# Optimization experiments

Hardware: AMD Instinct MI355X
Metric: run time of the kernel (lower is better)

The kernel has to match this reference:

```python
import jax, jax.numpy as jnp
import numpy as np

N_HEADS = 16
D_HEAD = 64


def setup_inputs() -> dict:
    key = jax.random.key(0)
    ks = jax.random.split(key, 9)
    B, n, L, Lt = 2, 8, 4096, 77
    d, ctx = 1024, 768
    H = W = 64
    s = 0.02  # weight init scale for numerical sanity
    return {
        "x": jax.random.normal(ks[0], (B, L, d), jnp.float32),
        "reorg_masks": jax.random.uniform(ks[1], (B, n, H, W), jnp.float32),
        "text_feat": jax.random.normal(ks[2], (B, n, Lt, ctx), jnp.float32),
        "Wq": jax.random.normal(ks[3], (d, d), jnp.float32) * s,
        "Wk": jax.random.normal(ks[4], (ctx, d), jnp.float32) * s,
        "Wv": jax.random.normal(ks[5], (ctx, d), jnp.float32) * s,
        "Wo": jax.random.normal(ks[6], (d, d), jnp.float32) * s,
        "bo": jax.random.normal(ks[7], (d,), jnp.float32) * s,
        "null_text_feat": jax.random.normal(ks[8], (d,), jnp.float32) * s,
    }


def _cross_attention(xf, ctx, Wq, Wk, Wv, Wo, bo):
    # xf: (BN, L, d), ctx: (BN, Lt, c)
    BN, L, _ = xf.shape
    Lt = ctx.shape[1]
    q = (xf @ Wq).reshape(BN, L, N_HEADS, D_HEAD)
    k = (ctx @ Wk).reshape(BN, Lt, N_HEADS, D_HEAD)
    v = (ctx @ Wv).reshape(BN, Lt, N_HEADS, D_HEAD)
    scale = 1.0 / np.sqrt(D_HEAD).astype(np.float32)
    logits = jnp.einsum("blhd,bthd->bhlt", q, k) * scale
    attn = jax.nn.softmax(logits, axis=-1)
    out = jnp.einsum("bhlt,bthd->blhd", attn, v).reshape(BN, L, N_HEADS * D_HEAD)
    return out @ Wo + bo


def reference(x, reorg_masks, text_feat, Wq, Wk, Wv, Wo, bo, null_text_feat):
    B, L, d = x.shape
    n = reorg_masks.shape[1]
    # masks are already at (H, W) with H*W == L, so nearest interp is identity
    x_flat = jnp.broadcast_to(x[:, None], (B, n, L, d)).reshape(B * n, L, d)
    ctx_flat = text_feat.reshape(B * n, text_feat.shape[2], text_feat.shape[3])
    x_obj = _cross_attention(x_flat, ctx_flat, Wq, Wk, Wv, Wo, bo)
    x_obj = x_obj.reshape(B, n, L, d)
    region = jnp.where(reorg_masks > 0.5, 1.0, 0.0).astype(x.dtype)
    region = region.reshape(B, n, L, 1)  # (b, n, h*w, 1)
    x_sum = jnp.sum(x_obj * region, axis=1)  # (B, L, d)
    cover = jnp.sum(region, axis=1)  # (B, L, 1)
    x_null = (1.0 - cover) * null_text_feat[None, None, :]
    return x_sum + x_null + x
```

## Files before the change

### kernel.cpp

```cpp
#include <hip/hip_runtime.h>


typedef __bf16 bf16;
typedef __bf16 bf16x8 __attribute__((ext_vector_type(8)));
typedef __bf16 bf16x4 __attribute__((ext_vector_type(4)));
typedef float  f32x4  __attribute__((ext_vector_type(4)));

#define MFMA16(a, b, c) __builtin_amdgcn_mfma_f32_16x16x32_bf16((a), (b), (c), 0, 0, 0)


__device__ inline bf16x8 cvt8(const float* p) {
  f32x4 a = *(const f32x4*)p;
  f32x4 b = *(const f32x4*)(p + 4);
  bf16x8 r;
  r[0] = (bf16)a[0]; r[1] = (bf16)a[1]; r[2] = (bf16)a[2]; r[3] = (bf16)a[3];
  r[4] = (bf16)b[0]; r[5] = (bf16)b[1]; r[6] = (bf16)b[2]; r[7] = (bf16)b[3];
  return r;
}

__global__ __launch_bounds__(256) void transpose_all(
    const float* __restrict__ Wq, const float* __restrict__ Wk,
    const float* __restrict__ Wv, const float* __restrict__ Wo,
    bf16* __restrict__ WqT, bf16* __restrict__ WkT,
    bf16* __restrict__ WvT, bf16* __restrict__ WoT,
    const float* __restrict__ mask, float* __restrict__ cover) {
  __shared__ bf16 tile[32][33];
  int bx = blockIdx.x;
  int byg = blockIdx.y;
  if (byg == 112) {
    int tid = bx * 256 + threadIdx.x;
    int b = tid >> 12, l = tid & 4095;
    float c = 0.f;
#pragma unroll
    for (int n = 0; n < 8; n++)
      c += (mask[(size_t)(b * 8 + n) * 4096 + l] > 0.5f) ? 1.f : 0.f;
    cover[tid] = c;
    return;
  }
  int tx = threadIdx.x & 31, ty = threadIdx.x >> 5;
  const float* in;
  bf16* out;
  int R, by;
  if (byg < 32)      { in = Wq; out = WqT; R = 1024; by = byg; }
  else if (byg < 56) { in = Wk; out = WkT; R = 768;  by = byg - 32; }
  else if (byg < 80) { in = Wv; out = WvT; R = 768;  by = byg - 56; }
  else               { in = Wo; out = WoT; R = 1024; by = byg - 80; }
  const int C = 1024;
  int c = bx * 32 + tx;
#pragma unroll
  for (int i = 0; i < 32; i += 8) {
    int r = by * 32 + ty + i;
    tile[ty + i][tx] = (bf16)in[(size_t)r * C + c];
  }
  __syncthreads();
#pragma unroll
  for (int i = 0; i < 32; i += 8) {
    out[(size_t)(bx * 32 + ty + i) * R + by * 32 + tx] = tile[tx][ty + i];
  }
}

__device__ __forceinline__ void gemm_q_body(const float* __restrict__ A,
                                            const bf16* __restrict__ BT,
                                            bf16* __restrict__ C,
                                            int bx, int by) {
  __shared__ __align__(16) bf16 asA[2][64 * 32];
  const int tid = threadIdx.x;
  const int lane = tid & 63, wave = tid >> 6;
  const int l16 = lane & 15, quad = lane >> 4;
  const int m0 = by * 64;
  const int n0 = bx * 256 + wave * 64;
  const int srow = tid >> 2, scol = (tid & 3) * 8;
  const float* aptr = A + (size_t)(m0 + srow) * 1024 + scol;

  *(bf16x8*)(&asA[0][srow * 32 + scol]) = cvt8(aptr);

  f32x4 acc[4][4];
#pragma unroll
  for (int i = 0; i < 4; i++)
#pragma unroll
    for (int j = 0; j < 4; j++)
#pragma unroll
      for (int r = 0; r < 4; r++) acc[i][j][r] = 0.f;

  for (int kt = 0; kt < 32; kt++) {
    bf16x8 wnext;
    if (kt + 1 < 32) wnext = cvt8(aptr + (kt + 1) * 32);
    __syncthreads();
    const bf16* ab = &asA[kt & 1][0];
    bf16x8 a[4], b[4];
#pragma unroll
    for (int mi = 0; mi < 4; mi++)
      a[mi] = *(const bf16x8*)(ab + (mi * 16 + l16) * 32 + quad * 8);
#pragma unroll
    for (int ni = 0; ni < 4; ni++)
      b[ni] = *(const bf16x8*)(BT + (size_t)(n0 + ni * 16 + l16) * 1024 + kt * 32 + quad * 8);
#pragma unroll
    for (int mi = 0; mi < 4; mi++)
#pragma unroll
      for (int ni = 0; ni < 4; ni++) acc[mi][ni] = MFMA16(a[mi], b[ni], acc[mi][ni]);
    if (kt + 1 < 32)
      *(bf16x8*)(&asA[(kt + 1) & 1][srow * 32 + scol]) = wnext;
  }

#pragma unroll
  for (int mi = 0; mi < 4; mi++)
#pragma unroll
    for (int r = 0; r < 4; r++) {
      int row = m0 + mi * 16 + quad * 4 + r;
#pragma unroll
      for (int ni = 0; ni < 4; ni++)
        C[(size_t)row * 1024 + n0 + ni * 16 + l16] = (bf16)(acc[mi][ni][r] * 0.125f);
    }
}

__device__ __forceinline__ void gemm_k_body(const float* __restrict__ text,
                                            const bf16* __restrict__ WkT,
                                            bf16* __restrict__ Kp,
                                            int bx, int bn) {
  const int tid = threadIdx.x;
  const int lane = tid & 63, wave = tid >> 6;
  const int l16 = lane & 15, quad = lane >> 4;
  const int m0 = (wave >> 1) * 64;
  const int n0 = bx * 128 + (wave & 1) * 64;
  const float* A = text + (size_t)bn * 77 * 768;
  bf16* dst = Kp + (size_t)bn * 80 * 1024;

  f32x4 acc[4][4];
#pragma unroll
  for (int i = 0; i < 4; i++)
#pragma unroll
    for (int j = 0; j < 4; j++)
#pragma unroll
      for (int r = 0; r < 4; r++) acc[i][j][r] = 0.f;

  for (int k0 = 0; k0 < 768; k0 += 32) {
    bf16x8 a[4], b[4];
#pragma unroll
    for (int mi = 0; mi < 4; mi++) {
      int row = m0 + mi * 16 + l16;
      if (row >= 77) row = 76;
      a[mi] = cvt8(A + (size_t)row * 768 + k0 + quad * 8);
    }
#pragma unroll
    for (int ni = 0; ni < 4; ni++)
      b[ni] = *(const bf16x8*)(WkT + (size_t)(n0 + ni * 16 + l16) * 768 + k0 + quad * 8);
#pragma unroll
    for (int mi = 0; mi < 4; mi++)
#pragma unroll
      for (int ni = 0; ni < 4; ni++) acc[mi][ni] = MFMA16(a[mi], b[ni], acc[mi][ni]);
  }

#pragma unroll
  for (int mi = 0; mi < 4; mi++)
#pragma unroll
    for (int r = 0; r < 4; r++) {
      int t = m0 + mi * 16 + quad * 4 + r;
      if (t < 77) {
#pragma unroll
        for (int ni = 0; ni < 4; ni++)
          dst[(size_t)t * 1024 + n0 + ni * 16 + l16] = (bf16)acc[mi][ni][r];
      } else if (t < 80) {
#pragma unroll
        for (int ni = 0; ni < 4; ni++)
          dst[(size_t)t * 1024 + n0 + ni * 16 + l16] = (bf16)0.f;
      }
    }
}

__device__ __forceinline__ void gemm_v_body(const float* __restrict__ text,
                                            const bf16* __restrict__ WvT,
                                            bf16* __restrict__ Vt,
                                            int bx, int bn) {
  const int tid = threadIdx.x;
  const int lane = tid & 63, wave = tid >> 6;
  const int l16 = lane & 15, quad = lane >> 4;
  const int m0 = (wave >> 1) * 64;
  const int n0 = bx * 128 + (wave & 1) * 64;
  const float* A = text + (size_t)bn * 77 * 768;
  bf16* dst = Vt + (size_t)bn * 1024 * 96;

  f32x4 acc[4][4];
#pragma unroll
  for (int i = 0; i < 4; i++)
#pragma unroll
    for (int j = 0; j < 4; j++)
#pragma unroll
      for (int r = 0; r < 4; r++) acc[i][j][r] = 0.f;

  for (int k0 = 0; k0 < 768; k0 += 32) {
    bf16x8 a[4], b[4];
#pragma unroll
    for (int mi = 0; mi < 4; mi++) {
      int row = m0 + mi * 16 + l16;
      if (row >= 77) row = 76;
      a[mi] = cvt8(A + (size_t)row * 768 + k0 + quad * 8);
    }
#pragma unroll
    for (int ni = 0; ni < 4; ni++)
      b[ni] = *(const bf16x8*)(WvT + (size_t)(n0 + ni * 16 + l16) * 768 + k0 + quad * 8);
#pragma unroll
    for (int mi = 0; mi < 4; mi++)
#pragma unroll
      for (int ni = 0; ni < 4; ni++) acc[mi][ni] = MFMA16(a[mi], b[ni], acc[mi][ni]);
  }

#pragma unroll
  for (int mi = 0; mi < 4; mi++) {
    int t0 = m0 + mi * 16 + quad * 4;
#pragma unroll
    for (int ni = 0; ni < 4; ni++) {
      int col = n0 + ni * 16 + l16;
      bf16* cbase = dst + (size_t)col * 96;
      if (t0 + 3 < 77) {
        bf16x4 w;
        w[0] = (bf16)acc[mi][ni][0]; w[1] = (bf16)acc[mi][ni][1];
        w[2] = (bf16)acc[mi][ni][2]; w[3] = (bf16)acc[mi][ni][3];
        *(bf16x4*)(cbase + t0) = w;
      } else {
#pragma unroll
        for (int r = 0; r < 4; r++) {
          int t = t0 + r;
          if (t < 77)      cbase[t] = (bf16)acc[mi][ni][r];
          else if (t < 96) cbase[t] = (bf16)0.f;
        }
      }
    }
  }
}

__global__ __launch_bounds__(256) void proj_qkv(const float* __restrict__ x,
                                                const bf16* __restrict__ WqT,
                                                bf16* __restrict__ Qb,
                                                const float* __restrict__ text,
                                                const bf16* __restrict__ WkT,
                                                const bf16* __restrict__ WvT,
                                                bf16* __restrict__ Kp,
                                                bf16* __restrict__ Vt) {
  const int bid = blockIdx.x;
  if (bid < 512) {
    gemm_q_body(x, WqT, Qb, bid & 3, bid >> 2);
  } else {
    const int r = bid - 512;
    const int bx = r & 7, bn = (r >> 3) & 15, kz = r >> 7;
    if (kz == 0) gemm_k_body(text, WkT, Kp, bx, bn);
    else         gemm_v_body(text, WvT, Vt, bx, bn);
  }
}

__global__ __launch_bounds__(256) void gemm_q_f(const float* __restrict__ A,
                                                const bf16* __restrict__ BT,
                                                float* __restrict__ C) {
  __shared__ __align__(16) bf16 asA[2][64 * 32];
  const int tid = threadIdx.x;
  const int lane = tid & 63, wave = tid >> 6;
  const int l16 = lane & 15, quad = lane >> 4;
  const int m0 = blockIdx.y * 64;
  const int n0 = blockIdx.x * 256 + wave * 64;
  const int srow = tid >> 2, scol = (tid & 3) * 8;
  const float* aptr = A + (size_t)(m0 + srow) * 1024 + scol;

  *(bf16x8*)(&asA[0][srow * 32 + scol]) = cvt8(aptr);

  f32x4 acc[4][4];
#pragma unroll
  for (int i = 0; i < 4; i++)
#pragma unroll
    for (int j = 0; j < 4; j++)
#pragma unroll
      for (int r = 0; r < 4; r++) acc[i][j][r] = 0.f;

  for (int kt = 0; kt < 32; kt++) {
    bf16x8 wnext;
    if (kt + 1 < 32) wnext = cvt8(aptr + (kt + 1) * 32);
    __syncthreads();
    const bf16* ab = &asA[kt & 1][0];
    bf16x8 a[4], b[4];
#pragma unroll
    for (int mi = 0; mi < 4; mi++)
      a[mi] = *(const bf16x8*)(ab + (mi * 16 + l16) * 32 + quad * 8);
#pragma unroll
    for (int ni = 0; ni < 4; ni++)
      b[ni] = *(const bf16x8*)(BT + (size_t)(n0 + ni * 16 + l16) * 1024 + kt * 32 + quad * 8);
#pragma unroll
    for (int mi = 0; mi < 4; mi++)
#pragma unroll
      for (int ni = 0; ni < 4; ni++) acc[mi][ni] = MFMA16(a[mi], b[ni], acc[mi][ni]);
    if (kt + 1 < 32) {
      *(bf16x8*)(&asA[(kt + 1) & 1][srow * 32 + scol]) = wnext;
    }
  }

#pragma unroll
  for (int mi = 0; mi < 4; mi++)
#pragma unroll
    for (int r = 0; r < 4; r++) {
      int row = m0 + mi * 16 + quad * 4 + r;
#pragma unroll
      for (int ni = 0; ni < 4; ni++)
        C[(size_t)row * 1024 + n0 + ni * 16 + l16] = acc[mi][ni][r] * 0.125f;
    }
}

template <typename OutT, typename InT>
__device__ __forceinline__ void attn_body(const InT* Qsrc, OutT* Odst,
                                          const bf16* __restrict__ Kp,
                                          const bf16* __restrict__ Vt,
                                          const float* __restrict__ mask) {
  __shared__ __align__(16) bf16 kl[80 * 72];
  __shared__ __align__(16) bf16 vl[64 * 104];
  __shared__ __align__(16) bf16 p_lds[4][16 * 104];
  const int tid = threadIdx.x;
  const int lane = tid & 63, wave = tid >> 6;
  const int l16 = lane & 15, quad = lane >> 4;
  const int bid = blockIdx.x;
  const int qg = bid & 31;
  const int h = (bid >> 5) & 15;
  const int b = bid >> 9;
  const int qrow0 = qg * 128 + wave * 32;
  bf16* pl = &p_lds[wave][0];

  for (int i = lane; i < 16 * 16; i += 64) {
    int r = i >> 4, c = 80 + (i & 15);
    pl[r * 104 + c] = (bf16)0.f;
  }

  bf16x8 qf[2][2];
#pragma unroll
  for (int mi = 0; mi < 2; mi++)
#pragma unroll
    for (int ks = 0; ks < 2; ks++) {
      const InT* qp = Qsrc + (size_t)(b * 4096 + qrow0 + mi * 16 + l16) * 1024 +
                      h * 64 + ks * 32 + quad * 8;
      if constexpr (sizeof(InT) == 4) qf[mi][ks] = cvt8((const float*)qp);
      else                            qf[mi][ks] = *(const bf16x8*)qp;
    }

  unsigned rbits[2];
#pragma unroll
  for (int mi = 0; mi < 2; mi++) {
    unsigned m = 0;
#pragma unroll
    for (int n = 0; n < 8; n++)
      if (mask[(size_t)(b * 8 + n) * 4096 + qrow0 + mi * 16 + l16] > 0.5f)
        m |= (1u << n);
    rbits[mi] = m;
  }

  f32x4 oacc[2][4];
#pragma unroll
  for (int mi = 0; mi < 2; mi++)
#pragma unroll
    for (int nt = 0; nt < 4; nt++)
#pragma unroll
      for (int r = 0; r < 4; r++) oacc[mi][nt][r] = 0.f;

  for (int n = 0; n < 8; n++) {
    const int bn = b * 8 + n;
    const bf16* Ksrc = Kp + (size_t)bn * 80 * 1024 + h * 64;
    const bf16* Vsrc = Vt + (size_t)bn * 1024 * 96 + (size_t)h * 64 * 96;

    for (int i = tid; i < 640; i += 256) {
      int row = i >> 3, c8 = (i & 7) * 8;
      *(bf16x8*)(kl + row * 72 + c8) = *(const bf16x8*)(Ksrc + (size_t)row * 1024 + c8);
    }
    for (int i = tid; i < 768; i += 256) {
      int row = i / 12, c8 = (i % 12) * 8;
      *(bf16x8*)(vl + row * 104 + c8) = *(const bf16x8*)(Vsrc + (size_t)row * 96 + c8);
    }
    __syncthreads();

    f32x4 s[2][5];
#pragma unroll
    for (int mi = 0; mi < 2; mi++)
#pragma unroll
      for (int tt = 0; tt < 5; tt++)
#pragma unroll
        for (int r = 0; r < 4; r++) s[mi][tt][r] = 0.f;

#pragma unroll
    for (int tt = 0; tt < 5; tt++) {
      int t = tt * 16 + l16;
      bf16x8 kf0 = *(const bf16x8*)(kl + t * 72 + quad * 8);
      bf16x8 kf1 = *(const bf16x8*)(kl + t * 72 + 32 + quad * 8);
#pragma unroll
      for (int mi = 0; mi < 2; mi++) {
        s[mi][tt] = MFMA16(kf0, qf[mi][0], s[mi][tt]);
        s[mi][tt] = MFMA16(kf1, qf[mi][1], s[mi][tt]);
      }
    }

#pragma unroll
    for (int mi = 0; mi < 2; mi++) {
      float sum = 0.f;
#pragma unroll
      for (int tt = 0; tt < 5; tt++) {
#pragma unroll
        for (int r = 0; r < 4; r++) {
          float e = __expf(s[mi][tt][r]);
          if (tt == 4 && quad * 4 + r >= 13) e = 0.f;
          s[mi][tt][r] = e;
          sum += e;
        }
      }
      sum += __shfl_xor(sum, 16);
      sum += __shfl_xor(sum, 32);
      float rg = ((rbits[mi] >> n) & 1u) ? 1.f : 0.f;
      float scale = rg / sum;
#pragma unroll
      for (int tt = 0; tt < 5; tt++) {
        bf16x4 w;
#pragma unroll
        for (int r = 0; r < 4; r++) w[r] = (bf16)(s[mi][tt][r] * scale);
        *(bf16x4*)(pl + l16 * 104 + tt * 16 + quad * 4) = w;
      }

#pragma unroll
      for (int ks = 0; ks < 3; ks++) {
        bf16x8 pf = *(const bf16x8*)(pl + l16 * 104 + ks * 32 + quad * 8);
#pragma unroll
        for (int nt = 0; nt < 4; nt++) {
          bf16x8 vf = *(const bf16x8*)(vl + (nt * 16 + l16) * 104 + ks * 32 + quad * 8);
          oacc[mi][nt] = MFMA16(pf, vf, oacc[mi][nt]);
        }
      }
    }
    __syncthreads();
  }

#pragma unroll
  for (int mi = 0; mi < 2; mi++)
#pragma unroll
    for (int r = 0; r < 4; r++) {
      size_t row = (size_t)(b * 4096 + qrow0 + mi * 16 + quad * 4 + r);
#pragma unroll
      for (int nt = 0; nt < 4; nt++)
        Odst[row * 1024 + h * 64 + nt * 16 + l16] = (OutT)oacc[mi][nt][r];
    }
}

__global__ __launch_bounds__(256, 4) void attn_b(const bf16* Qb, bf16* ACCb,
                                                 const bf16* __restrict__ Kp,
                                                 const bf16* __restrict__ Vt,
                                                 const float* __restrict__ mask) {
  attn_body<bf16, bf16>(Qb, ACCb, Kp, Vt, mask);
}
__global__ __launch_bounds__(256, 4) void attn_f(float* QO,
                                                 const bf16* __restrict__ Kp,
                                                 const bf16* __restrict__ Vt,
                                                 const float* __restrict__ mask) {
  attn_body<float, float>(QO, QO, Kp, Vt, mask);
}

__global__ __launch_bounds__(256) void gemm_wo_ep2(const bf16* __restrict__ A,
                                                   const bf16* __restrict__ BT,
                                                   const float* __restrict__ x,
                                                   const float* __restrict__ bo,
                                                   const float* __restrict__ nullf,
                                                   const float* __restrict__ cover,
                                                   float* __restrict__ out) {
  __shared__ __align__(16) bf16 asA[2][128 * 32];
  const int tid = threadIdx.x;
  const int lane = tid & 63, wave = tid >> 6;
  const int l16 = lane & 15, quad = lane >> 4;
  const int mb = blockIdx.y * 128;
  const int m0 = mb + (wave >> 1) * 64;
  const int n0 = blockIdx.x * 128 + (wave & 1) * 64;
  const int r0 = (tid * 2) >> 2, c0 = ((tid * 2) & 3) * 8;
  const int r1 = (tid * 2 + 1) >> 2, c1 = ((tid * 2 + 1) & 3) * 8;

  *(bf16x8*)(&asA[0][r0 * 32 + c0]) = *(const bf16x8*)(A + (size_t)(mb + r0) * 1024 + c0);
  *(bf16x8*)(&asA[0][r1 * 32 + c1]) = *(const bf16x8*)(A + (size_t)(mb + r1) * 1024 + c1);

  f32x4 acc[4][4];
#pragma unroll
  for (int i = 0; i < 4; i++)
#pragma unroll
    for (int j = 0; j < 4; j++)
#pragma unroll
      for (int r = 0; r < 4; r++) acc[i][j][r] = 0.f;

  for (int kt = 0; kt < 32; kt++) {
    bf16x8 p0, p1;
    if (kt + 1 < 32) {
      p0 = *(const bf16x8*)(A + (size_t)(mb + r0) * 1024 + (kt + 1) * 32 + c0);
      p1 = *(const bf16x8*)(A + (size_t)(mb + r1) * 1024 + (kt + 1) * 32 + c1);
    }
    __syncthreads();
    const bf16* ab = &asA[kt & 1][0];
    bf16x8 a[4], b[4];
#pragma unroll
    for (int mi = 0; mi < 4; mi++)
      a[mi] = *(const bf16x8*)(ab + ((wave >> 1) * 64 + mi * 16 + l16) * 32 + quad * 8);
#pragma unroll
    for (int ni = 0; ni < 4; ni++)
      b[ni] = *(const bf16x8*)(BT + (size_t)(n0 + ni * 16 + l16) * 1024 + kt * 32 + quad * 8);
#pragma unroll
    for (int mi = 0; mi < 4; mi++)
#pragma unroll
      for (int ni = 0; ni < 4; ni++) acc[mi][ni] = MFMA16(a[mi], b[ni], acc[mi][ni]);
    if (kt + 1 < 32) {
      *(bf16x8*)(&asA[(kt + 1) & 1][r0 * 32 + c0]) = p0;
      *(bf16x8*)(&asA[(kt + 1) & 1][r1 * 32 + c1]) = p1;
    }
  }

#pragma unroll
  for (int mi = 0; mi < 4; mi++)
#pragma unroll
    for (int r = 0; r < 4; r++) {
      int row = m0 + mi * 16 + quad * 4 + r;
      float cv = cover[row];
#pragma unroll
      for (int ni = 0; ni < 4; ni++) {
        int col = n0 + ni * 16 + l16;
        float v = acc[mi][ni][r] + cv * bo[col] + (1.f - cv) * nullf[col] +
                  x[(size_t)row * 1024 + col];
        out[(size_t)row * 1024 + col] = v;
      }
    }
}

__global__ __launch_bounds__(512) void gemm_wo_ep(float* QO,
                                                  const bf16* __restrict__ WoT,
                                                  const float* __restrict__ x,
                                                  const float* __restrict__ bo,
                                                  const float* __restrict__ nullf,
                                                  const float* __restrict__ cover) {
  __shared__ __align__(16) bf16 lds_a[32 * 32 * 32];
  const int tid = threadIdx.x;
  const int lane = tid & 63, wv = tid >> 6;
  const int l16 = lane & 15, quad = lane >> 4;
  const int m0 = blockIdx.x * 32;

#pragma unroll
  for (int c = 0; c < 16; c++) {
    int ch = c * 512 + tid;
    int row = ch >> 8;
    int pos4 = (ch & 255) * 4;
    int kt = pos4 >> 5, kin = pos4 & 31;
    f32x4 v = *(const f32x4*)(QO + (size_t)(m0 + row) * 1024 + pos4);
    bf16x4 w;
    w[0] = (bf16)v[0]; w[1] = (bf16)v[1]; w[2] = (bf16)v[2]; w[3] = (bf16)v[3];
    *(bf16x4*)(lds_a + kt * 1024 + row * 32 + kin) = w;
  }
  __syncthreads();

  const int n0 = wv * 128;
  f32x4 acc[2][8];
#pragma unroll
  for (int mi = 0; mi < 2; mi++)
#pragma unroll
    for (int ni = 0; ni < 8; ni++)
#pragma unroll
      for (int r = 0; r < 4; r++) acc[mi][ni][r] = 0.f;

  for (int kt = 0; kt < 32; kt++) {
    bf16x8 a[2];
#pragma unroll
    for (int mi = 0; mi < 2; mi++)
      a[mi] = *(const bf16x8*)(lds_a + kt * 1024 + (mi * 16 + l16) * 32 + quad * 8);
    bf16x8 bfr[8];
#pragma unroll
    for (int ni = 0; ni < 8; ni++)
      bfr[ni] = *(const bf16x8*)(WoT + (size_t)(n0 + ni * 16 + l16) * 1024 + kt * 32 + quad * 8);
#pragma unroll
    for (int mi = 0; mi < 2; mi++)
#pragma unroll
      for (int ni = 0; ni < 8; ni++) acc[mi][ni] = MFMA16(a[mi], bfr[ni], acc[mi][ni]);
  }

#pragma unroll
  for (int mi = 0; mi < 2; mi++)
#pragma unroll
    for (int r = 0; r < 4; r++) {
      int row = m0 + mi * 16 + quad * 4 + r;
      float cv = cover[row];
#pragma unroll
      for (int ni = 0; ni < 8; ni++) {
        int col = n0 + ni * 16 + l16;
        float v = acc[mi][ni][r] + cv * bo[col] + (1.f - cv) * nullf[col] +
                  x[(size_t)row * 1024 + col];
        QO[(size_t)row * 1024 + col] = v;
      }
    }
}

extern "C" void kernel_launch(void* const* d_in, const int* in_sizes, int n_in,
                              void* d_out, int out_size, void* d_ws, size_t ws_size,
                              hipStream_t stream) {
  const float* x     = (const float*)d_in[0];
  const float* masks = (const float*)d_in[1];
  const float* text  = (const float*)d_in[2];
  const float* Wq    = (const float*)d_in[3];
  const float* Wk    = (const float*)d_in[4];
  const float* Wv    = (const float*)d_in[5];
  const float* Wo    = (const float*)d_in[6];
  const float* bo    = (const float*)d_in[7];
  const float* nullf = (const float*)d_in[8];
  float* out = (float*)d_out;

  bf16* ws  = (bf16*)d_ws;
  bf16* WqT = ws;
  bf16* WkT = WqT + 1048576;
  bf16* WvT = WkT + 786432;
  bf16* WoT = WvT + 786432;
  bf16* Kp  = WoT + 1048576;
  bf16* Vt  = Kp + 1310720;
  float* cover = (float*)(Vt + 1572864);
  bf16* ACCb = (bf16*)(cover + 8192);
  const size_t NEEDED = 13139968 + 16777216;

  transpose_all<<<dim3(32, 113), 256, 0, stream>>>(Wq, Wk, Wv, Wo, WqT, WkT, WvT, WoT,
                                                   masks, cover);

  if (ws_size >= NEEDED) {
    bf16* Qb = (bf16*)d_out;
    proj_qkv<<<768, 256, 0, stream>>>(x, WqT, Qb, text, WkT, WvT, Kp, Vt);
    attn_b<<<1024, 256, 0, stream>>>(Qb, ACCb, Kp, Vt, masks);
    gemm_wo_ep2<<<dim3(8, 64), 256, 0, stream>>>(ACCb, WoT, x, bo, nullf, cover, out);
  } else {
    proj_qkv<<<768, 256, 0, stream>>>(x, WqT, (bf16*)d_ws , text, WkT, WvT, Kp, Vt);
    gemm_q_f<<<dim3(4, 128), 256, 0, stream>>>(x, WqT, out);
    attn_f<<<1024, 256, 0, stream>>>(out, Kp, Vt, masks);
    gemm_wo_ep<<<256, 512, 0, stream>>>(out, WoT, x, bo, nullf, cover);
  }
}
```

Measured before the change: 288.2 us.

## Load Q-GEMM A operand directly from global, reorder PV MFMAs, trim fallback launch

The Q projection GEMMs stop staging the fp32 A tile in LDS with double buffering and barriers. Each wave now loads and converts its A fragments straight from global memory, removing __syncthreads at the cost of redundant global reads across the four waves. The attention PV step first loads all P fragments for both row tiles and then reuses each V fragment for two MFMAs, halving V LDS reads. The fallback path also drops the redundant Q blocks from proj_qkv via a new qcount argument.

```diff
diff --git a/kernel.cpp b/kernel.cpp
--- a/kernel.cpp
+++ b/kernel.cpp
@@ -63,16 +63,11 @@
                                             const bf16* __restrict__ BT,
                                             bf16* __restrict__ C,
                                             int bx, int by) {
-  __shared__ __align__(16) bf16 asA[2][64 * 32];
   const int tid = threadIdx.x;
   const int lane = tid & 63, wave = tid >> 6;
   const int l16 = lane & 15, quad = lane >> 4;
   const int m0 = by * 64;
   const int n0 = bx * 256 + wave * 64;
-  const int srow = tid >> 2, scol = (tid & 3) * 8;
-  const float* aptr = A + (size_t)(m0 + srow) * 1024 + scol;
-
-  *(bf16x8*)(&asA[0][srow * 32 + scol]) = cvt8(aptr);
 
   f32x4 acc[4][4];
 #pragma unroll
@@ -83,14 +78,10 @@
       for (int r = 0; r < 4; r++) acc[i][j][r] = 0.f;
 
   for (int kt = 0; kt < 32; kt++) {
-    bf16x8 wnext;
-    if (kt + 1 < 32) wnext = cvt8(aptr + (kt + 1) * 32);
-    __syncthreads();
-    const bf16* ab = &asA[kt & 1][0];
     bf16x8 a[4], b[4];
 #pragma unroll
     for (int mi = 0; mi < 4; mi++)
-      a[mi] = *(const bf16x8*)(ab + (mi * 16 + l16) * 32 + quad * 8);
+      a[mi] = cvt8(A + (size_t)(m0 + mi * 16 + l16) * 1024 + kt * 32 + quad * 8);
 #pragma unroll
     for (int ni = 0; ni < 4; ni++)
       b[ni] = *(const bf16x8*)(BT + (size_t)(n0 + ni * 16 + l16) * 1024 + kt * 32 + quad * 8);
@@ -98,8 +89,6 @@
     for (int mi = 0; mi < 4; mi++)
 #pragma unroll
       for (int ni = 0; ni < 4; ni++) acc[mi][ni] = MFMA16(a[mi], b[ni], acc[mi][ni]);
-    if (kt + 1 < 32)
-      *(bf16x8*)(&asA[(kt + 1) & 1][srow * 32 + scol]) = wnext;
   }
 
 #pragma unroll
@@ -235,12 +224,13 @@
                                                 const bf16* __restrict__ WkT,
                                                 const bf16* __restrict__ WvT,
                                                 bf16* __restrict__ Kp,
-                                                bf16* __restrict__ Vt) {
+                                                bf16* __restrict__ Vt,
+                                                int qcount) {
   const int bid = blockIdx.x;
-  if (bid < 512) {
+  if (bid < qcount) {
     gemm_q_body(x, WqT, Qb, bid & 3, bid >> 2);
   } else {
-    const int r = bid - 512;
+    const int r = bid - qcount;
     const int bx = r & 7, bn = (r >> 3) & 15, kz = r >> 7;
     if (kz == 0) gemm_k_body(text, WkT, Kp, bx, bn);
     else         gemm_v_body(text, WvT, Vt, bx, bn);
@@ -250,16 +240,11 @@
 __global__ __launch_bounds__(256) void gemm_q_f(const float* __restrict__ A,
                                                 const bf16* __restrict__ BT,
                                                 float* __restrict__ C) {
-  __shared__ __align__(16) bf16 asA[2][64 * 32];
   const int tid = threadIdx.x;
   const int lane = tid & 63, wave = tid >> 6;
   const int l16 = lane & 15, quad = lane >> 4;
   const int m0 = blockIdx.y * 64;
   const int n0 = blockIdx.x * 256 + wave * 64;
-  const int srow = tid >> 2, scol = (tid & 3) * 8;
-  const float* aptr = A + (size_t)(m0 + srow) * 1024 + scol;
-
-  *(bf16x8*)(&asA[0][srow * 32 + scol]) = cvt8(aptr);
 
   f32x4 acc[4][4];
 #pragma unroll
@@ -270,14 +255,10 @@
       for (int r = 0; r < 4; r++) acc[i][j][r] = 0.f;
 
   for (int kt = 0; kt < 32; kt++) {
-    bf16x8 wnext;
-    if (kt + 1 < 32) wnext = cvt8(aptr + (kt + 1) * 32);
-    __syncthreads();
-    const bf16* ab = &asA[kt & 1][0];
     bf16x8 a[4], b[4];
 #pragma unroll
     for (int mi = 0; mi < 4; mi++)
-      a[mi] = *(const bf16x8*)(ab + (mi * 16 + l16) * 32 + quad * 8);
+      a[mi] = cvt8(A + (size_t)(m0 + mi * 16 + l16) * 1024 + kt * 32 + quad * 8);
 #pragma unroll
     for (int ni = 0; ni < 4; ni++)
       b[ni] = *(const bf16x8*)(BT + (size_t)(n0 + ni * 16 + l16) * 1024 + kt * 32 + quad * 8);
@@ -285,9 +266,6 @@
     for (int mi = 0; mi < 4; mi++)
 #pragma unroll
       for (int ni = 0; ni < 4; ni++) acc[mi][ni] = MFMA16(a[mi], b[ni], acc[mi][ni]);
-    if (kt + 1 < 32) {
-      *(bf16x8*)(&asA[(kt + 1) & 1][srow * 32 + scol]) = wnext;
-    }
   }
 
 #pragma unroll
@@ -389,6 +367,7 @@
       }
     }
 
+    bf16x8 pfr[2][3];
 #pragma unroll
     for (int mi = 0; mi < 2; mi++) {
       float sum = 0.f;
@@ -413,15 +392,18 @@
         for (int r = 0; r < 4; r++) w[r] = (bf16)(s[mi][tt][r] * scale);
         *(bf16x4*)(pl + l16 * 104 + tt * 16 + quad * 4) = w;
       }
-
-#pragma unroll
-      for (int ks = 0; ks < 3; ks++) {
-        bf16x8 pf = *(const bf16x8*)(pl + l16 * 104 + ks * 32 + quad * 8);
-#pragma unroll
-        for (int nt = 0; nt < 4; nt++) {
-          bf16x8 vf = *(const bf16x8*)(vl + (nt * 16 + l16) * 104 + ks * 32 + quad * 8);
-          oacc[mi][nt] = MFMA16(pf, vf, oacc[mi][nt]);
-        }
+#pragma unroll
+      for (int ks = 0; ks < 3; ks++)
+        pfr[mi][ks] = *(const bf16x8*)(pl + l16 * 104 + ks * 32 + quad * 8);
+    }
+
+#pragma unroll
+    for (int ks = 0; ks < 3; ks++) {
+#pragma unroll
+      for (int nt = 0; nt < 4; nt++) {
+        bf16x8 vf = *(const bf16x8*)(vl + (nt * 16 + l16) * 104 + ks * 32 + quad * 8);
+        oacc[0][nt] = MFMA16(pfr[0][ks], vf, oacc[0][nt]);
+        oacc[1][nt] = MFMA16(pfr[1][ks], vf, oacc[1][nt]);
       }
     }
     __syncthreads();
@@ -615,11 +597,11 @@
 
   if (ws_size >= NEEDED) {
     bf16* Qb = (bf16*)d_out;
-    proj_qkv<<<768, 256, 0, stream>>>(x, WqT, Qb, text, WkT, WvT, Kp, Vt);
+    proj_qkv<<<768, 256, 0, stream>>>(x, WqT, Qb, text, WkT, WvT, Kp, Vt, 512);
     attn_b<<<1024, 256, 0, stream>>>(Qb, ACCb, Kp, Vt, masks);
     gemm_wo_ep2<<<dim3(8, 64), 256, 0, stream>>>(ACCb, WoT, x, bo, nullf, cover, out);
   } else {
-    proj_qkv<<<768, 256, 0, stream>>>(x, WqT, (bf16*)d_ws , text, WkT, WvT, Kp, Vt);
+    proj_qkv<<<256, 256, 0, stream>>>(x, WqT, nullptr, text, WkT, WvT, Kp, Vt, 0);
     gemm_q_f<<<dim3(4, 128), 256, 0, stream>>>(x, WqT, out);
     attn_f<<<1024, 256, 0, stream>>>(out, Kp, Vt, masks);
     gemm_wo_ep<<<256, 512, 0, stream>>>(out, WoT, x, bo, nullf, cover);
```

Result: slower. 318.7 us (+10.6%).
